# Performance work log

Measured on AMD Instinct MI355X. Metric: run time of the kernel, lower is better.

## Reference

```python
import jax, jax.numpy as jnp
import numpy as np

B, S, C, H, E, K = 8, 512, 768, 12, 8, 2
MLP_H = int(C * 4.0)
HD = C // H
ROUTER_REG = 0.01
LN_EPS = 1e-5


def setup_inputs() -> dict:
    key = jax.random.key(0)
    ks = jax.random.split(key, 8)

    def w(k, shape, fan_in):
        return (jax.random.normal(k, shape, dtype=jnp.float32) / np.sqrt(fan_in)).astype(jnp.float32)

    return {
        "x": jax.random.normal(ks[0], (B, S, C), dtype=jnp.float32),
        "expert_tokens": w(ks[1], (E, C), C),
        "ln1_g": jnp.ones((E, C), jnp.float32),
        "ln1_b": jnp.zeros((E, C), jnp.float32),
        "qkv_w": w(ks[2], (E, C, 3 * C), C),
        "qkv_b": jnp.zeros((E, 3 * C), jnp.float32),
        "proj_w": w(ks[3], (E, C, C), C),
        "proj_b": jnp.zeros((E, C), jnp.float32),
        "ln2_g": jnp.ones((E, C), jnp.float32),
        "ln2_b": jnp.zeros((E, C), jnp.float32),
        "fc1_w": w(ks[4], (E, C, MLP_H), C),
        "fc1_b": jnp.zeros((E, MLP_H), jnp.float32),
        "fc2_w": w(ks[5], (E, MLP_H, C), MLP_H),
        "fc2_b": jnp.zeros((E, C), jnp.float32),
    }


def _layernorm(x, g, b):
    mu = jnp.mean(x, axis=-1, keepdims=True)
    var = jnp.mean(jnp.square(x - mu), axis=-1, keepdims=True)
    return (x - mu) * jax.lax.rsqrt(var + LN_EPS) * g + b


def _block(x, p):
    # One transformer Block (pre-LN attention + MLP), params for a single expert.
    ln1_g, ln1_b, qkv_w, qkv_b, proj_w, proj_b, ln2_g, ln2_b, fc1_w, fc1_b, fc2_w, fc2_b = p
    h = _layernorm(x, ln1_g, ln1_b)
    qkv = (h @ qkv_w + qkv_b).reshape(B, S, 3, H, HD)
    q, k, v = qkv[:, :, 0], qkv[:, :, 1], qkv[:, :, 2]  # [B,S,H,HD]
    # NOTE: original code MULTIPLIES by sqrt(head_dim) (scale = head_dim**0.5).
    scale = jnp.float32(np.sqrt(HD))
    attn = jax.nn.softmax(jnp.einsum('bqhd,bkhd->bhqk', q, k) * scale, axis=-1)
    o = jnp.einsum('bhqk,bkhd->bqhd', attn, v).reshape(B, S, C)
    x = x + (o @ proj_w + proj_b)
    h2 = _layernorm(x, ln2_g, ln2_b)
    x = x + (jax.nn.gelu(h2 @ fc1_w + fc1_b, approximate=False) @ fc2_w + fc2_b)
    return x


def reference(x, expert_tokens, ln1_g, ln1_b, qkv_w, qkv_b, proj_w, proj_b,
              ln2_g, ln2_b, fc1_w, fc1_b, fc2_w, fc2_b):
    # Router
    router_logits = jnp.einsum('bsc,nc->bsn', x, expert_tokens) / jnp.float32(np.sqrt(C))
    router_probs = jax.nn.softmax(router_logits, axis=-1)
    top_k_probs, top_k_idx = jax.lax.top_k(router_probs, K)  # [B,S,K]
    top_k_probs = top_k_probs / jnp.sum(top_k_probs, axis=-1, keepdims=True)

    # Dense all-expert compute (sequential over experts to bound memory)
    params = (ln1_g, ln1_b, qkv_w, qkv_b, proj_w, proj_b, ln2_g, ln2_b,
              fc1_w, fc1_b, fc2_w, fc2_b)
    expert_out = jax.lax.map(lambda p: _block(x, p), params)  # [E,B,S,C]
    expert_out = jnp.transpose(expert_out, (1, 2, 0, 3))       # [B,S,E,C]

    # Top-k gather and weighted combine
    sel = jnp.take_along_axis(expert_out, top_k_idx[..., None], axis=2)  # [B,S,K,C]
    combine = jnp.sum(sel * top_k_probs[..., None], axis=2)
    out = x + combine

    # Load-balance auxiliary loss
    counts = jnp.sum(jax.nn.one_hot(top_k_idx, E, dtype=jnp.float32), axis=(0, 1, 2))
    f_i = counts / jnp.float32(B * S * K)
    P_i = jnp.mean(router_probs, axis=(0, 1))
    balance_loss = E * jnp.sum(f_i * P_i) + ROUTER_REG * jnp.linalg.norm(expert_tokens)
    return out, balance_loss
```

## Files before the change

### kernel.cpp

```cpp
#include <hip/hip_runtime.h>
#include <hip/hip_bf16.h>

#define BB 8
#define SS 512
#define CC 768
#define HH 12
#define HD 64
#define EE 8
#define KK 2
#define MLPH 3072
#define NT (BB*SS)
#define NOUT (NT*CC)

#define SLOTB      68059136ull
#define SLOT_U16   34029568ull
#define SLOT_F32   17014784ull

typedef unsigned int u32;
typedef unsigned short u16;
typedef __attribute__((ext_vector_type(8))) short short8;
typedef __attribute__((ext_vector_type(4))) float f32x4;

__device__ __forceinline__ u16 f2bf(float f) {
    u32 u = __builtin_bit_cast(u32, f);
    u32 r = (u + 0x7fffu + ((u >> 16) & 1u)) >> 16;
    return (u16)r;
}
__device__ __forceinline__ float bf2f(u16 h) {
    u32 u = ((u32)h) << 16;
    return __builtin_bit_cast(float, u);
}
__device__ __forceinline__ void gl_lds16(const void* g, void* l) {
    __builtin_amdgcn_global_load_lds(
        (const __attribute__((address_space(1))) u32*)g,
        (__attribute__((address_space(3))) u32*)l, 16, 0, 0);
}
__device__ __forceinline__ void swz_rc(int bid, int& bm, int& bn) {
    int xcd = bid & 7, off = bid >> 3;
    bm = (xcd * 4 + (off & 3)) * 128;
    bn = (off >> 2) * 128;
}

__device__ __forceinline__ void stage128x64(const u16* __restrict__ G, size_t ldg,
                                            u16* s, int tid)
{
    int wid = tid >> 6, lane = tid & 63;
#pragma unroll
    for (int it = 0; it < 4; ++it) {
        int cb = it * 256 + wid * 64;
        int c = cb + lane;
        int row = c >> 3;
        int ch = (c & 7) ^ (row & 7);
        gl_lds16(G + (size_t)row * ldg + ch * 8, s + cb * 8);
    }
}
__device__ __forceinline__ short8 frag64(const u16* s, int row, int kc, int lb) {
    int ch = (kc * 4 + lb) ^ (row & 7);
    return *(const short8*)(s + row * 64 + ch * 8);
}

__device__ __forceinline__ void stg_dp(const u16* __restrict__ A, const u16* __restrict__ B,
                                       int ldk, u16* sA, u16* sB, int t, int tid)
{
    int wid = tid >> 6, lane = tid & 63;
#pragma unroll
    for (int rd = 0; rd < 2; rd++) {
        int cb = rd * 256 + wid * 64;
        int c = cb + lane;
        gl_lds16(A + (size_t)(c >> 2) * ldk + t * 32 + (c & 3) * 8, sA + cb * 8);
    }
#pragma unroll
    for (int rd = 0; rd < 2; rd++) {
        int cb = rd * 256 + wid * 64;
        int c = cb + lane;
        gl_lds16(B + (size_t)(c >> 2) * ldk + t * 32 + (c & 3) * 8, sB + cb * 8);
    }
}

__global__ __launch_bounds__(256) void router_kernel(const float* __restrict__ x,
    const float* __restrict__ et, float* __restrict__ W, float* __restrict__ stats)
{
    __shared__ float etl[EE * CC];
    __shared__ float pred[4][2 * EE];
    int tid = threadIdx.x;
    for (int i = tid; i < EE * CC; i += 256) etl[i] = et[i];
    __syncthreads();
    int wid = tid >> 6, lane = tid & 63;
    float psum[EE] = {}, csum[EE] = {};
    for (int i = 0; i < 2; i++) {
        int t = blockIdx.x * 8 + wid * 2 + i;
        const float* xr = x + (size_t)t * CC;
        float acc[EE] = {};
        for (int c = lane; c < CC; c += 64) {
            float xv = xr[c];
#pragma unroll
            for (int e = 0; e < EE; e++) acc[e] += xv * etl[e * CC + c];
        }
#pragma unroll
        for (int e = 0; e < EE; e++)
            for (int off = 1; off < 64; off <<= 1) acc[e] += __shfl_xor(acc[e], off, 64);
        if (lane == 0) {
            const float inv = 0.03608439182435161f;
            float l[EE], m = -1e30f;
#pragma unroll
            for (int e = 0; e < EE; e++) { l[e] = acc[e] * inv; m = fmaxf(m, l[e]); }
            float p[EE], sum = 0.f;
#pragma unroll
            for (int e = 0; e < EE; e++) { p[e] = __expf(l[e] - m); sum += p[e]; }
            int i1 = 0;
#pragma unroll
            for (int e = 1; e < EE; e++) if (p[e] > p[i1]) i1 = e;
            int i2 = -1;
#pragma unroll
            for (int e = 0; e < EE; e++) if (e != i1 && (i2 < 0 || p[e] > p[i2])) i2 = e;
            float wn = p[i1] + p[i2];
#pragma unroll
            for (int e = 0; e < EE; e++) W[t * EE + e] = 0.f;
            W[t * EE + i1] = p[i1] / wn;
            W[t * EE + i2] = p[i2] / wn;
#pragma unroll
            for (int e = 0; e < EE; e++) psum[e] += p[e] / sum;
            csum[i1] += 1.f; csum[i2] += 1.f;
        }
    }
    if (lane == 0) {
#pragma unroll
        for (int e = 0; e < EE; e++) { pred[wid][e] = psum[e]; pred[wid][EE + e] = csum[e]; }
    }
    __syncthreads();
    if (tid < 2 * EE) {
        float s = pred[0][tid] + pred[1][tid] + pred[2][tid] + pred[3][tid];
        atomicAdd(&stats[tid], s);
    }
}

template<int MODE>
__global__ __launch_bounds__(256) void ln_kernel(const float* __restrict__ x, size_t xslot,
    u16* __restrict__ out_hi, u16* __restrict__ out_lo, size_t oslot)
{
    int t = blockIdx.x;
    int eb = blockIdx.y;
    const float* xr = x + (size_t)eb * xslot + (size_t)t * CC;
    __shared__ float red[256];
    int tid = threadIdx.x;
    float v[3];
    float s = 0.f;
#pragma unroll
    for (int i = 0; i < 3; i++) { v[i] = xr[tid + i * 256]; s += v[i]; }
    red[tid] = s; __syncthreads();
    for (int off = 128; off > 0; off >>= 1) { if (tid < off) red[tid] += red[tid + off]; __syncthreads(); }
    float mu = red[0] / (float)CC;
    __syncthreads();
    float s2 = 0.f;
#pragma unroll
    for (int i = 0; i < 3; i++) { float d = v[i] - mu; s2 += d * d; }
    red[tid] = s2; __syncthreads();
    for (int off = 128; off > 0; off >>= 1) { if (tid < off) red[tid] += red[tid + off]; __syncthreads(); }
    float var = red[0] / (float)CC;
    float sc = rsqrtf(var + 1e-5f);
#pragma unroll
    for (int i = 0; i < 3; i++) {
        int c = tid + i * 256;
        float val = (v[i] - mu) * sc;
        u16 hi = f2bf(val);
        out_hi[(size_t)eb * oslot + (size_t)t * CC + c] = hi;
        if (MODE) out_lo[(size_t)eb * oslot + (size_t)t * CC + c] = f2bf(val - bf2f(hi));
    }
}

__global__ __launch_bounds__(256) void prep_expert(
    const float* __restrict__ qkv_w0, const float* __restrict__ qkv_b0,
    const float* __restrict__ proj_w0,
    const float* __restrict__ fc1_w0, const float* __restrict__ fc1_b0,
    const float* __restrict__ fc2_w0,
    const float* __restrict__ g1_0, const float* __restrict__ b1_0,
    const float* __restrict__ g2_0, const float* __restrict__ b2_0,
    u16* __restrict__ qkvTh, u16* __restrict__ qkvTl,
    u16* __restrict__ projT, u16* __restrict__ fc1T, u16* __restrict__ fc2T,
    float* __restrict__ biasq, float* __restrict__ biasf1, int ebase)
{
    __shared__ float tile[32][33];
    __shared__ float bsh[CC];
    __shared__ float redg[256];
    int bid = blockIdx.x;
    int eb = blockIdx.y;
    int ge = ebase + eb;
    int tid = threadIdx.x;
    const float* qkv_w = qkv_w0 + (size_t)ge * CC * 3 * CC;
    const float* qkv_b = qkv_b0 + (size_t)ge * 3 * CC;
    const float* proj_w = proj_w0 + (size_t)ge * CC * CC;
    const float* fc1_w = fc1_w0 + (size_t)ge * CC * MLPH;
    const float* fc1_b = fc1_b0 + (size_t)ge * MLPH;
    const float* fc2_w = fc2_w0 + (size_t)ge * MLPH * CC;
    const float* g1 = g1_0 + (size_t)ge * CC;
    const float* b1 = b1_0 + (size_t)ge * CC;
    const float* g2 = g2_0 + (size_t)ge * CC;
    const float* b2 = b2_0 + (size_t)ge * CC;

    if (bid < 6912) {
        const float* src; const float* scale = nullptr;
        u16 *dh, *dl = nullptr; int N, Kd, n0, k0;
        if (bid < 1728) {
            src = qkv_w; scale = g1;
            dh = qkvTh + (size_t)eb * SLOT_U16; dl = qkvTl + (size_t)eb * SLOT_U16;
            N = 2304; Kd = 768; n0 = (bid % 72) * 32; k0 = (bid / 72) * 32;
        } else if (bid < 2304) {
            int i = bid - 1728;
            src = proj_w; dh = projT + (size_t)eb * SLOT_U16; N = 768; Kd = 768;
            n0 = (i % 24) * 32; k0 = (i / 24) * 32;
        } else if (bid < 4608) {
            int i = bid - 2304;
            src = fc1_w; scale = g2; dh = fc1T + (size_t)eb * SLOT_U16; N = 3072; Kd = 768;
            n0 = (i % 96) * 32; k0 = (i / 96) * 32;
        } else {
            int i = bid - 4608;
            src = fc2_w; dh = fc2T + (size_t)eb * SLOT_U16; N = 768; Kd = 3072;
            n0 = (i % 24) * 32; k0 = (i / 24) * 32;
        }
        int tx = tid & 31, ty = tid >> 5;
#pragma unroll
        for (int i = 0; i < 32; i += 8) {
            float v = src[(size_t)(k0 + ty + i) * N + n0 + tx];
            if (scale) v *= scale[k0 + ty + i];
            tile[ty + i][tx] = v;
        }
        __syncthreads();
#pragma unroll
        for (int i = 0; i < 32; i += 8) {
            float v = tile[tx][ty + i];
            u16 hi = f2bf(v);
            dh[(size_t)(n0 + ty + i) * Kd + k0 + tx] = hi;
            if (dl) dl[(size_t)(n0 + ty + i) * Kd + k0 + tx] = f2bf(v - bf2f(hi));
        }
    } else {
        const float* bv; const float* wsrc; const float* badd;
        float* dst; int N, n0;
        if (bid < 6984) { bv = b1; wsrc = qkv_w; badd = qkv_b; dst = biasq + (size_t)eb * SLOT_F32; N = 2304; n0 = (bid - 6912) * 32; }
        else            { bv = b2; wsrc = fc1_w; badd = fc1_b; dst = biasf1 + (size_t)eb * SLOT_F32; N = MLPH; n0 = (bid - 6984) * 32; }
        for (int i = tid; i < CC; i += 256) bsh[i] = bv[i];
        __syncthreads();
        int g = tid & 31, l8 = tid >> 5;
        int n = n0 + g;
        float acc = 0.f;
        for (int k = l8; k < CC; k += 8) acc += bsh[k] * wsrc[(size_t)k * N + n];
        redg[tid] = acc; __syncthreads();
        if (tid < 32) {
            float sum = 0.f;
#pragma unroll
            for (int i = 0; i < 8; i++) sum += redg[tid + i * 32];
            dst[n0 + tid] = sum + badd[n0 + tid];
        }
    }
}

__global__ __launch_bounds__(256) void gemm_qkv_bk64(
    const u16* __restrict__ Ah, const u16* __restrict__ Al,
    const u16* __restrict__ Bh0, const u16* __restrict__ Bl0,
    const float* __restrict__ biasq0, u16* __restrict__ qk_hi0,
    u16* __restrict__ qk_lo0, u16* __restrict__ vtout0)
{
    __shared__ __align__(16) u16 sAh[128 * 64], sAl[128 * 64];
    __shared__ __align__(16) u16 sBh[128 * 64], sBl[128 * 64];
    int tid = threadIdx.x;
    int eb = blockIdx.y;
    int bm, bn;
    swz_rc(blockIdx.x, bm, bn);
    bool qk_tile = (bn < 1536);
    int wid = tid >> 6, lane = tid & 63;
    int wr = wid >> 1, wc = wid & 1;
    int la = lane & 15, lb = lane >> 4;
    const u16* Bh = Bh0 + (size_t)eb * SLOT_U16;
    const u16* Bl = Bl0 + (size_t)eb * SLOT_U16;
    const float* bias = biasq0 + (size_t)eb * SLOT_F32;
    u16* qk_hi = qk_hi0 + (size_t)eb * SLOT_U16;
    u16* qk_lo = qk_lo0 + (size_t)eb * SLOT_U16;
    u16* vtout = vtout0 + (size_t)eb * SLOT_U16;

    f32x4 acc[4][4];
#pragma unroll
    for (int i = 0; i < 4; i++)
#pragma unroll
        for (int j = 0; j < 4; j++) acc[i][j] = (f32x4){0.f, 0.f, 0.f, 0.f};

    const u16* Abh = Ah + (size_t)bm * CC;
    const u16* Abl = Al + (size_t)bm * CC;
    const u16* Bbh = Bh + (size_t)bn * CC;
    const u16* Bbl = Bl + (size_t)bn * CC;
    for (int k0 = 0; k0 < CC; k0 += 64) {
        stage128x64(Abh + k0, CC, sAh, tid);
        stage128x64(Bbh + k0, CC, sBh, tid);
        if (qk_tile) {
            stage128x64(Abl + k0, CC, sAl, tid);
            stage128x64(Bbl + k0, CC, sBl, tid);
        }
        __syncthreads();
        if (qk_tile) {
#pragma unroll
            for (int kc = 0; kc < 2; kc++) {
                short8 avh[4], avl[4], bvh[4], bvl[4];
#pragma unroll
                for (int i = 0; i < 4; i++) {
                    int row = wr * 64 + i * 16 + la;
                    avh[i] = frag64(sAh, row, kc, lb);
                    avl[i] = frag64(sAl, row, kc, lb);
                }
#pragma unroll
                for (int j = 0; j < 4; j++) {
                    int row = wc * 64 + j * 16 + la;
                    bvh[j] = frag64(sBh, row, kc, lb);
                    bvl[j] = frag64(sBl, row, kc, lb);
                }
#pragma unroll
                for (int i = 0; i < 4; i++)
#pragma unroll
                    for (int j = 0; j < 4; j++) {
                        acc[i][j] = __builtin_amdgcn_mfma_f32_16x16x32_bf16(avh[i], bvh[j], acc[i][j], 0, 0, 0);
                        acc[i][j] = __builtin_amdgcn_mfma_f32_16x16x32_bf16(avh[i], bvl[j], acc[i][j], 0, 0, 0);
                        acc[i][j] = __builtin_amdgcn_mfma_f32_16x16x32_bf16(avl[i], bvh[j], acc[i][j], 0, 0, 0);
                    }
            }
        } else {
#pragma unroll
            for (int kc = 0; kc < 2; kc++) {
                short8 avh[4], bvh[4];
#pragma unroll
                for (int i = 0; i < 4; i++) avh[i] = frag64(sAh, wr * 64 + i * 16 + la, kc, lb);
#pragma unroll
                for (int j = 0; j < 4; j++) bvh[j] = frag64(sBh, wc * 64 + j * 16 + la, kc, lb);
#pragma unroll
                for (int i = 0; i < 4; i++)
#pragma unroll
                    for (int j = 0; j < 4; j++)
                        acc[i][j] = __builtin_amdgcn_mfma_f32_16x16x32_bf16(avh[i], bvh[j], acc[i][j], 0, 0, 0);
            }
        }
        __syncthreads();
    }
#pragma unroll
    for (int i = 0; i < 4; i++) {
#pragma unroll
        for (int j = 0; j < 4; j++) {
            int gn = bn + wc * 64 + j * 16 + la;
            float bsv = bias[gn];
#pragma unroll
            for (int r = 0; r < 4; r++) {
                int gm = bm + wr * 64 + i * 16 + lb * 4 + r;
                float v = acc[i][j][r] + bsv;
                if (gn < 1536) {
                    u16 hi = f2bf(v);
                    qk_hi[(size_t)gm * 1536 + gn] = hi;
                    qk_lo[(size_t)gm * 1536 + gn] = f2bf(v - bf2f(hi));
                } else {
                    int dd = (gn - 1536) & 63, hh = (gn - 1536) >> 6;
                    int ss = gm & (SS - 1), bb = gm >> 9;
                    vtout[((size_t)((bb * HH + hh) * HD + dd)) * SS + ss] = f2bf(v);
                }
            }
        }
    }
}

__global__ __launch_bounds__(256) void gemm_proj(
    const u16* __restrict__ A, const u16* __restrict__ BT,
    const float* __restrict__ bias0, const float* __restrict__ x,
    float* __restrict__ Cout)
{
    __shared__ __align__(16) u16 sA[128 * 64];
    __shared__ __align__(16) u16 sB[128 * 64];
    int tid = threadIdx.x;
    int eb = blockIdx.y;
    int bm, bn;
    swz_rc(blockIdx.x, bm, bn);
    int wid = tid >> 6, lane = tid & 63;
    int wr = wid >> 1, wc = wid & 1;
    int la = lane & 15, lb = lane >> 4;
    f32x4 acc[4][4];
#pragma unroll
    for (int i = 0; i < 4; i++)
#pragma unroll
        for (int j = 0; j < 4; j++) acc[i][j] = (f32x4){0.f, 0.f, 0.f, 0.f};

    const u16* Ab = A + (size_t)eb * SLOT_U16 + (size_t)bm * CC;
    const u16* Bb = BT + (size_t)eb * SLOT_U16 + (size_t)bn * CC;
    for (int k0 = 0; k0 < CC; k0 += 64) {
        stage128x64(Ab + k0, CC, sA, tid);
        stage128x64(Bb + k0, CC, sB, tid);
        __syncthreads();
#pragma unroll
        for (int kc = 0; kc < 2; kc++) {
            short8 av[4], bv[4];
#pragma unroll
            for (int i = 0; i < 4; i++) av[i] = frag64(sA, wr * 64 + i * 16 + la, kc, lb);
#pragma unroll
            for (int j = 0; j < 4; j++) bv[j] = frag64(sB, wc * 64 + j * 16 + la, kc, lb);
#pragma unroll
            for (int i = 0; i < 4; i++)
#pragma unroll
                for (int j = 0; j < 4; j++)
                    acc[i][j] = __builtin_amdgcn_mfma_f32_16x16x32_bf16(av[i], bv[j], acc[i][j], 0, 0, 0);
        }
        __syncthreads();
    }
    const float* biasp = bias0 + (size_t)eb * CC;
    float* C = Cout + (size_t)eb * SLOT_F32;
#pragma unroll
    for (int i = 0; i < 4; i++) {
#pragma unroll
        for (int j = 0; j < 4; j++) {
            int gn = bn + wc * 64 + j * 16 + la;
            float bsv = biasp[gn];
#pragma unroll
            for (int r = 0; r < 4; r++) {
                int gm = bm + wr * 64 + i * 16 + lb * 4 + r;
                size_t idx = (size_t)gm * CC + gn;
                C[idx] = x[idx] + acc[i][j][r] + bsv;
            }
        }
    }
}

template<int EPI>
__device__ __forceinline__ void gemm_dp_body(
    const u16* __restrict__ Ab, const u16* __restrict__ Bb, int Kdim,
    const float* __restrict__ biasp, const float* __restrict__ resp,
    const float* __restrict__ Wt, int ge, const float* __restrict__ xinit,
    void* __restrict__ Cout, int N, int bm, int bn)
{
    __shared__ __align__(16) u16 sA[3][128 * 32];
    __shared__ __align__(16) u16 sB[3][128 * 32];
    int tid = threadIdx.x;
    int wid = tid >> 6, lane = tid & 63;
    int wr = wid >> 1, wc = wid & 1;
    int la = lane & 15, lb = lane >> 4;
    int NTILE = Kdim / 32;

    f32x4 acc[4][4];
#pragma unroll
    for (int i = 0; i < 4; i++)
#pragma unroll
        for (int j = 0; j < 4; j++) acc[i][j] = (f32x4){0.f, 0.f, 0.f, 0.f};

    stg_dp(Ab, Bb, Kdim, sA[0], sB[0], 0, tid);
    stg_dp(Ab, Bb, Kdim, sA[1], sB[1], 1, tid);

    for (int t = 0; t < NTILE; t++) {
        if (t < NTILE - 1) asm volatile("s_waitcnt vmcnt(4)" ::: "memory");
        else               asm volatile("s_waitcnt vmcnt(0)" ::: "memory");
        asm volatile("" ::: "memory");
        __builtin_amdgcn_s_barrier();
        asm volatile("" ::: "memory");

        const u16* cA = &sA[t % 3][0];
        const u16* cB = &sB[t % 3][0];
        __builtin_amdgcn_s_setprio(1);
        short8 bv[4];
#pragma unroll
        for (int j = 0; j < 4; j++)
            bv[j] = *(const short8*)(cB + ((size_t)(wc * 64 + j * 16 + la) * 4 + lb) * 8);
#pragma unroll
        for (int i = 0; i < 4; i++) {
            short8 av = *(const short8*)(cA + ((size_t)(wr * 64 + i * 16 + la) * 4 + lb) * 8);
#pragma unroll
            for (int j = 0; j < 4; j++)
                acc[i][j] = __builtin_amdgcn_mfma_f32_16x16x32_bf16(av, bv[j], acc[i][j], 0, 0, 0);
        }
        __builtin_amdgcn_s_setprio(0);

        if (t + 2 < NTILE) stg_dp(Ab, Bb, Kdim, sA[(t + 2) % 3], sB[(t + 2) % 3], t + 2, tid);
    }

#pragma unroll
    for (int i = 0; i < 4; i++) {
#pragma unroll
        for (int j = 0; j < 4; j++) {
            int gn = bn + wc * 64 + j * 16 + la;
            float bsv = biasp[gn];
#pragma unroll
            for (int r = 0; r < 4; r++) {
                int gm = bm + wr * 64 + i * 16 + lb * 4 + r;
                size_t idx = (size_t)gm * N + gn;
                float v = acc[i][j][r] + bsv;
                if (EPI == 2) {
                    float gel = 0.5f * v * (1.0f + erff(v * 0.70710678118654752f));
                    ((u16*)Cout)[idx] = f2bf(gel);
                } else {
                    float w = Wt[(size_t)gm * EE + ge];
                    float val = w * (v + resp[idx]);
                    if (ge == 0) val += xinit[idx];
                    atomicAdd(&((float*)Cout)[idx], val);
                }
            }
        }
    }
}

__global__ __launch_bounds__(256) void gemm_fc1_dp(
    const u16* __restrict__ A0, const u16* __restrict__ BT0,
    const float* __restrict__ bias0, u16* __restrict__ C0)
{
    int eb = blockIdx.y;
    int bm, bn;
    swz_rc(blockIdx.x, bm, bn);
    gemm_dp_body<2>(A0 + (size_t)eb * SLOT_U16 + (size_t)bm * CC,
                    BT0 + (size_t)eb * SLOT_U16 + (size_t)bn * CC, CC,
                    bias0 + (size_t)eb * SLOT_F32, nullptr, nullptr, 0, nullptr,
                    C0 + (size_t)eb * SLOT_U16, MLPH, bm, bn);
}

__global__ __launch_bounds__(256) void gemm_fc2_dp(
    const u16* __restrict__ A0, const u16* __restrict__ BT0,
    const float* __restrict__ bias0, const float* __restrict__ res0,
    const float* __restrict__ Wt, int ebase, const float* __restrict__ xinit,
    float* __restrict__ Cout)
{
    int eb = blockIdx.y;
    int bm, bn;
    swz_rc(blockIdx.x, bm, bn);
    gemm_dp_body<5>(A0 + (size_t)eb * SLOT_U16 + (size_t)bm * MLPH,
                    BT0 + (size_t)eb * SLOT_U16 + (size_t)bn * MLPH, MLPH,
                    bias0 + (size_t)eb * CC, res0 + (size_t)eb * SLOT_F32,
                    Wt, ebase + eb, xinit, Cout, CC, bm, bn);
}

__global__ __launch_bounds__(256) void attn_mfma(const u16* __restrict__ qk_hi0,
    const u16* __restrict__ qk_lo0, const u16* __restrict__ vt0, u16* __restrict__ o0)
{
    int q0 = blockIdx.x * 64;
    int h = blockIdx.y;
    int z = blockIdx.z;
    int b = z & (BB - 1), eb = z >> 3;
    int tid = threadIdx.x, wid = tid >> 6, lane = tid & 63;
    int la = lane & 15, lb = lane >> 4;
    __shared__ __align__(16) u16 Ksh[64 * 64];
    __shared__ __align__(16) u16 Ksl[64 * 64];
    __shared__ __align__(16) u16 Vs[64 * 64];
    __shared__ __align__(16) u16 Ps[4][16 * 64];

    const u16* qk_hi = qk_hi0 + (size_t)eb * SLOT_U16;
    const u16* qk_lo = qk_lo0 + (size_t)eb * SLOT_U16;
    const u16* vt = vt0 + (size_t)eb * SLOT_U16;
    u16* o = o0 + (size_t)eb * SLOT_U16;

    short8 aqh[2], aql[2];
    {
        size_t qoff = (size_t)(b * SS + q0 + wid * 16 + la) * 1536 + h * HD;
#pragma unroll
        for (int kc = 0; kc < 2; kc++) {
            aqh[kc] = *(const short8*)(qk_hi + qoff + kc * 32 + lb * 8);
            aql[kc] = *(const short8*)(qk_lo + qoff + kc * 32 + lb * 8);
        }
    }
    const u16* kbh = qk_hi + (size_t)(b * SS) * 1536 + CC + h * HD;
    const u16* kbl = qk_lo + (size_t)(b * SS) * 1536 + CC + h * HD;
    const u16* vtbase = vt + (size_t)((b * HH + h) * HD) * SS;

    float m_r[4], l_r[4];
    f32x4 acc_o[4];
#pragma unroll
    for (int r = 0; r < 4; r++) { m_r[r] = -1e30f; l_r[r] = 0.f; }
#pragma unroll
    for (int d0 = 0; d0 < 4; d0++) acc_o[d0] = (f32x4){0.f, 0.f, 0.f, 0.f};

    for (int kt = 0; kt < SS; kt += 64) {
#pragma unroll
        for (int it = 0; it < 2; it++) {
            int base = it * 256 + wid * 64;
            int c = base + lane;
            int row = c >> 3;
            int gk = (c & 7) ^ (row & 7);
            gl_lds16(kbh + (size_t)(kt + row) * 1536 + gk * 8, Ksh + base * 8);
            gl_lds16(kbl + (size_t)(kt + row) * 1536 + gk * 8, Ksl + base * 8);
            gl_lds16(vtbase + (size_t)row * SS + kt + gk * 8, Vs + base * 8);
        }
        __syncthreads();

        f32x4 s4[4];
#pragma unroll
        for (int j = 0; j < 4; j++) s4[j] = (f32x4){0.f, 0.f, 0.f, 0.f};
#pragma unroll
        for (int kc = 0; kc < 2; kc++)
#pragma unroll
            for (int j = 0; j < 4; j++) {
                size_t off = (size_t)(j * 16 + la) * 64 + (((kc * 4 + lb) ^ (la & 7)) * 8);
                short8 bkh = *(const short8*)(Ksh + off);
                short8 bkl = *(const short8*)(Ksl + off);
                s4[j] = __builtin_amdgcn_mfma_f32_16x16x32_bf16(aqh[kc], bkh, s4[j], 0, 0, 0);
                s4[j] = __builtin_amdgcn_mfma_f32_16x16x32_bf16(aql[kc], bkh, s4[j], 0, 0, 0);
                s4[j] = __builtin_amdgcn_mfma_f32_16x16x32_bf16(aqh[kc], bkl, s4[j], 0, 0, 0);
            }
#pragma unroll
        for (int j = 0; j < 4; j++) s4[j] = s4[j] * 8.f;

#pragma unroll
        for (int r = 0; r < 4; r++) {
            float mx = fmaxf(fmaxf(s4[0][r], s4[1][r]), fmaxf(s4[2][r], s4[3][r]));
#pragma unroll
            for (int off = 1; off < 16; off <<= 1) mx = fmaxf(mx, __shfl_xor(mx, off, 64));
            float mn = fmaxf(m_r[r], mx);
            float corr = __expf(m_r[r] - mn);
            m_r[r] = mn;
            float rs = 0.f;
#pragma unroll
            for (int j = 0; j < 4; j++) {
                float p = __expf(s4[j][r] - mn);
                s4[j][r] = p; rs += p;
            }
#pragma unroll
            for (int off = 1; off < 16; off <<= 1) rs += __shfl_xor(rs, off, 64);
            l_r[r] = l_r[r] * corr + rs;
#pragma unroll
            for (int d0 = 0; d0 < 4; d0++) acc_o[d0][r] = acc_o[d0][r] * corr;
        }
#pragma unroll
        for (int j = 0; j < 4; j++)
#pragma unroll
            for (int r = 0; r < 4; r++) {
                int row = lb * 4 + r;
                int sg = (2 * j + (la >> 3)) ^ (row & 7);
                Ps[wid][row * 64 + sg * 8 + (la & 7)] = f2bf(s4[j][r]);
            }
        short8 pa[2];
#pragma unroll
        for (int kc = 0; kc < 2; kc++)
            pa[kc] = *(const short8*)(&Ps[wid][la * 64 + (((kc * 4 + lb) ^ (la & 7)) * 8)]);
#pragma unroll
        for (int d0 = 0; d0 < 4; d0++)
#pragma unroll
            for (int kc = 0; kc < 2; kc++) {
                short8 bv = *(const short8*)(&Vs[(d0 * 16 + la) * 64 + (((kc * 4 + lb) ^ (la & 7)) * 8)]);
                acc_o[d0] = __builtin_amdgcn_mfma_f32_16x16x32_bf16(pa[kc], bv, acc_o[d0], 0, 0, 0);
            }
        __syncthreads();
    }
#pragma unroll
    for (int r = 0; r < 4; r++) {
        float invl = 1.f / l_r[r];
        int tok = b * SS + q0 + wid * 16 + lb * 4 + r;
#pragma unroll
        for (int d0 = 0; d0 < 4; d0++)
            o[(size_t)tok * CC + h * HD + d0 * 16 + la] = f2bf(acc_o[d0][r] * invl);
    }
}

__global__ __launch_bounds__(256) void loss_kernel(const float* __restrict__ et,
    const float* __restrict__ stats, float* __restrict__ out_loss)
{
    __shared__ float red[256];
    int tid = threadIdx.x;
    float s = 0.f;
    for (int i = tid; i < EE * CC; i += 256) { float v = et[i]; s += v * v; }
    red[tid] = s; __syncthreads();
    for (int off = 128; off > 0; off >>= 1) { if (tid < off) red[tid] += red[tid + off]; __syncthreads(); }
    if (tid == 0) {
        float bl = 0.f;
        for (int e = 0; e < EE; e++) {
            float f = stats[EE + e] / (float)(NT * KK);
            float P = stats[e] / (float)NT;
            bl += f * P;
        }
        *out_loss = (float)EE * bl + 0.01f * sqrtf(red[0]);
    }
}

extern "C" void kernel_launch(void* const* d_in, const int* in_sizes, int n_in,
                              void* d_out, int out_size, void* d_ws, size_t ws_size,
                              hipStream_t stream) {
    const float* x      = (const float*)d_in[0];
    const float* et     = (const float*)d_in[1];
    const float* ln1_g  = (const float*)d_in[2];
    const float* ln1_b  = (const float*)d_in[3];
    const float* qkv_w  = (const float*)d_in[4];
    const float* qkv_b  = (const float*)d_in[5];
    const float* proj_w = (const float*)d_in[6];
    const float* proj_b = (const float*)d_in[7];
    const float* ln2_g  = (const float*)d_in[8];
    const float* ln2_b  = (const float*)d_in[9];
    const float* fc1_w  = (const float*)d_in[10];
    const float* fc1_b  = (const float*)d_in[11];
    const float* fc2_w  = (const float*)d_in[12];
    const float* fc2_b  = (const float*)d_in[13];
    float* outp = (float*)d_out;
    char* base = (char*)d_ws;

    const size_t FIXED = 12714496;
    int EB = 1;
    if (ws_size >= FIXED + 8 * SLOTB) EB = 8;
    else if (ws_size >= FIXED + 4 * SLOTB) EB = 4;
    else if (ws_size >= FIXED + 2 * SLOTB) EB = 2;

    float* W      = (float*)(base);
    float* stats  = (float*)(base + 131072);
    u16*   xh_hi  = (u16*)  (base + 131584);
    u16*   xh_lo  = (u16*)  (base + 6423040);
    char* slot0 = base + FIXED;
    u16*   qkvTh  = (u16*)  (slot0);
    u16*   qkvTl  = (u16*)  (slot0 + 3538944);
    u16*   projT  = (u16*)  (slot0 + 7077888);
    u16*   fc1T   = (u16*)  (slot0 + 8257536);
    u16*   fc2T   = (u16*)  (slot0 + 12976128);
    float* biasq  = (float*)(slot0 + 17694720);
    float* biasf1 = (float*)(slot0 + 17711104);
    u16*   qk_hi  = (u16*)  (slot0 + 17727488);
    u16*   qk_lo  = (u16*)  (slot0 + 30310400);
    u16*   mlp1   = (u16*)  (slot0 + 17727488);
    u16*   vtb    = (u16*)  (slot0 + 42893312);
    u16*   xmhat  = (u16*)  (slot0 + 42893312);
    u16*   obf    = (u16*)  (slot0 + 49184768);
    float* xmid   = (float*)(slot0 + 55476224);

    hipMemsetAsync(stats, 0, 16 * sizeof(float), stream);
    hipMemsetAsync(outp, 0, (size_t)NOUT * sizeof(float), stream);

    router_kernel<<<NT / 8, 256, 0, stream>>>(x, et, W, stats);
    ln_kernel<1><<<dim3(NT, 1), 256, 0, stream>>>(x, 0, xh_hi, xh_lo, 0);

    for (int ebase = 0; ebase < EE; ebase += EB) {
        prep_expert<<<dim3(7080, EB), 256, 0, stream>>>(
            qkv_w, qkv_b, proj_w, fc1_w, fc1_b, fc2_w,
            ln1_g, ln1_b, ln2_g, ln2_b,
            qkvTh, qkvTl, projT, fc1T, fc2T, biasq, biasf1, ebase);

        gemm_qkv_bk64<<<dim3(18 * 32, EB), 256, 0, stream>>>(
            xh_hi, xh_lo, qkvTh, qkvTl, biasq, qk_hi, qk_lo, vtb);

        attn_mfma<<<dim3(SS / 64, HH, BB * EB), 256, 0, stream>>>(qk_hi, qk_lo, vtb, obf);

        gemm_proj<<<dim3(6 * 32, EB), 256, 0, stream>>>(
            obf, projT, proj_b + (size_t)ebase * CC, x, xmid);

        ln_kernel<0><<<dim3(NT, EB), 256, 0, stream>>>(xmid, SLOT_F32, xmhat, nullptr, SLOT_U16);

        gemm_fc1_dp<<<dim3(24 * 32, EB), 256, 0, stream>>>(xmhat, fc1T, biasf1, mlp1);

        gemm_fc2_dp<<<dim3(6 * 32, EB), 256, 0, stream>>>(
            mlp1, fc2T, fc2_b + (size_t)ebase * CC, xmid, W, ebase, x, outp);
    }

    loss_kernel<<<1, 256, 0, stream>>>(et, stats, outp + NOUT);
}
```

Baseline: 1.448 ms.

## Pipeline QKV and proj GEMMs with triple-buffered async LDS staging

Replaces the single-buffered BK=64 QKV GEMM with a three-stage BK=32 pipeline using global_load_lds and vmcnt waits. B tiles are staged in LDS, while A fragments (hi/lo) are read directly from global memory into registers. The proj GEMM is moved onto the shared pipelined gemm_dp_body through a new EPI==1 residual epilogue. This aims to overlap loads with MFMA work and remove the per-tile double barrier, at the cost of uncached direct global reads for A, which are repeated across column tiles.

```diff
diff --git a/kernel.cpp b/kernel.cpp
--- a/kernel.cpp
+++ b/kernel.cpp
@@ -39,24 +39,6 @@
     int xcd = bid & 7, off = bid >> 3;
     bm = (xcd * 4 + (off & 3)) * 128;
     bn = (off >> 2) * 128;
-}
-
-__device__ __forceinline__ void stage128x64(const u16* __restrict__ G, size_t ldg,
-                                            u16* s, int tid)
-{
-    int wid = tid >> 6, lane = tid & 63;
-#pragma unroll
-    for (int it = 0; it < 4; ++it) {
-        int cb = it * 256 + wid * 64;
-        int c = cb + lane;
-        int row = c >> 3;
-        int ch = (c & 7) ^ (row & 7);
-        gl_lds16(G + (size_t)row * ldg + ch * 8, s + cb * 8);
-    }
-}
-__device__ __forceinline__ short8 frag64(const u16* s, int row, int kc, int lb) {
-    int ch = (kc * 4 + lb) ^ (row & 7);
-    return *(const short8*)(s + row * 64 + ch * 8);
 }
 
 __device__ __forceinline__ void stg_dp(const u16* __restrict__ A, const u16* __restrict__ B,
@@ -253,89 +235,106 @@
     }
 }
 
-__global__ __launch_bounds__(256) void gemm_qkv_bk64(
+__global__ __launch_bounds__(256) void gemm_qkv_dp(
     const u16* __restrict__ Ah, const u16* __restrict__ Al,
     const u16* __restrict__ Bh0, const u16* __restrict__ Bl0,
     const float* __restrict__ biasq0, u16* __restrict__ qk_hi0,
     u16* __restrict__ qk_lo0, u16* __restrict__ vtout0)
 {
-    __shared__ __align__(16) u16 sAh[128 * 64], sAl[128 * 64];
-    __shared__ __align__(16) u16 sBh[128 * 64], sBl[128 * 64];
+    __shared__ __align__(16) u16 sBh[3][128 * 32];
+    __shared__ __align__(16) u16 sBl[3][128 * 32];
+    const int NTILE = CC / 32;
     int tid = threadIdx.x;
     int eb = blockIdx.y;
     int bm, bn;
     swz_rc(blockIdx.x, bm, bn);
-    bool qk_tile = (bn < 1536);
+    bool qk = (bn < 1536);
     int wid = tid >> 6, lane = tid & 63;
     int wr = wid >> 1, wc = wid & 1;
     int la = lane & 15, lb = lane >> 4;
-    const u16* Bh = Bh0 + (size_t)eb * SLOT_U16;
-    const u16* Bl = Bl0 + (size_t)eb * SLOT_U16;
+
+    const u16* Bh = Bh0 + (size_t)eb * SLOT_U16 + (size_t)bn * CC;
+    const u16* Bl = Bl0 + (size_t)eb * SLOT_U16 + (size_t)bn * CC;
+    const u16* Ahb = Ah + (size_t)bm * CC;
+    const u16* Alb = Al + (size_t)bm * CC;
+
+    auto STG = [&](int s, int t) {
+#pragma unroll
+        for (int rd = 0; rd < 2; rd++) {
+            int cb = rd * 256 + wid * 64;
+            int c = cb + lane;
+            gl_lds16(Bh + (size_t)(c >> 2) * CC + t * 32 + (c & 3) * 8, &sBh[s][(size_t)cb * 8]);
+        }
+        if (qk) {
+#pragma unroll
+            for (int rd = 0; rd < 2; rd++) {
+                int cb = rd * 256 + wid * 64;
+                int c = cb + lane;
+                gl_lds16(Bl + (size_t)(c >> 2) * CC + t * 32 + (c & 3) * 8, &sBl[s][(size_t)cb * 8]);
+            }
+        }
+    };
+
+    f32x4 acc[4][4];
+#pragma unroll
+    for (int i = 0; i < 4; i++)
+#pragma unroll
+        for (int j = 0; j < 4; j++) acc[i][j] = (f32x4){0.f, 0.f, 0.f, 0.f};
+
+    STG(0, 0);
+    STG(1, 1);
+
+    for (int t = 0; t < NTILE; t++) {
+        if (t < NTILE - 1) {
+            if (qk) asm volatile("s_waitcnt vmcnt(4)" ::: "memory");
+            else    asm volatile("s_waitcnt vmcnt(2)" ::: "memory");
+        } else {
+            asm volatile("s_waitcnt vmcnt(0)" ::: "memory");
+        }
+        __builtin_amdgcn_s_barrier();
+        asm volatile("" ::: "memory");
+
+        short8 avh[4], avl[4];
+#pragma unroll
+        for (int i = 0; i < 4; i++)
+            avh[i] = *(const short8*)(Ahb + (size_t)(wr * 64 + i * 16 + la) * CC + t * 32 + lb * 8);
+        if (qk) {
+#pragma unroll
+            for (int i = 0; i < 4; i++)
+                avl[i] = *(const short8*)(Alb + (size_t)(wr * 64 + i * 16 + la) * CC + t * 32 + lb * 8);
+        }
+
+        const u16* cBh = &sBh[t % 3][0];
+        const u16* cBl = &sBl[t % 3][0];
+        __builtin_amdgcn_s_setprio(1);
+#pragma unroll
+        for (int j = 0; j < 4; j++) {
+            short8 bvh = *(const short8*)(cBh + (size_t)(wc * 64 + j * 16 + la) * 32 + lb * 8);
+#pragma unroll
+            for (int i = 0; i < 4; i++)
+                acc[i][j] = __builtin_amdgcn_mfma_f32_16x16x32_bf16(avh[i], bvh, acc[i][j], 0, 0, 0);
+        }
+        if (qk) {
+#pragma unroll
+            for (int j = 0; j < 4; j++) {
+                short8 bvh = *(const short8*)(cBh + (size_t)(wc * 64 + j * 16 + la) * 32 + lb * 8);
+                short8 bvl = *(const short8*)(cBl + (size_t)(wc * 64 + j * 16 + la) * 32 + lb * 8);
+#pragma unroll
+                for (int i = 0; i < 4; i++) {
+                    acc[i][j] = __builtin_amdgcn_mfma_f32_16x16x32_bf16(avh[i], bvl, acc[i][j], 0, 0, 0);
+                    acc[i][j] = __builtin_amdgcn_mfma_f32_16x16x32_bf16(avl[i], bvh, acc[i][j], 0, 0, 0);
+                }
+            }
+        }
+        __builtin_amdgcn_s_setprio(0);
+
+        if (t + 2 < NTILE) STG((t + 2) % 3, t + 2);
+    }
+
     const float* bias = biasq0 + (size_t)eb * SLOT_F32;
     u16* qk_hi = qk_hi0 + (size_t)eb * SLOT_U16;
     u16* qk_lo = qk_lo0 + (size_t)eb * SLOT_U16;
     u16* vtout = vtout0 + (size_t)eb * SLOT_U16;
-
-    f32x4 acc[4][4];
-#pragma unroll
-    for (int i = 0; i < 4; i++)
-#pragma unroll
-        for (int j = 0; j < 4; j++) acc[i][j] = (f32x4){0.f, 0.f, 0.f, 0.f};
-
-    const u16* Abh = Ah + (size_t)bm * CC;
-    const u16* Abl = Al + (size_t)bm * CC;
-    const u16* Bbh = Bh + (size_t)bn * CC;
-    const u16* Bbl = Bl + (size_t)bn * CC;
-    for (int k0 = 0; k0 < CC; k0 += 64) {
-        stage128x64(Abh + k0, CC, sAh, tid);
-        stage128x64(Bbh + k0, CC, sBh, tid);
-        if (qk_tile) {
-            stage128x64(Abl + k0, CC, sAl, tid);
-            stage128x64(Bbl + k0, CC, sBl, tid);
-        }
-        __syncthreads();
-        if (qk_tile) {
-#pragma unroll
-            for (int kc = 0; kc < 2; kc++) {
-                short8 avh[4], avl[4], bvh[4], bvl[4];
-#pragma unroll
-                for (int i = 0; i < 4; i++) {
-                    int row = wr * 64 + i * 16 + la;
-                    avh[i] = frag64(sAh, row, kc, lb);
-                    avl[i] = frag64(sAl, row, kc, lb);
-                }
-#pragma unroll
-                for (int j = 0; j < 4; j++) {
-                    int row = wc * 64 + j * 16 + la;
-                    bvh[j] = frag64(sBh, row, kc, lb);
-                    bvl[j] = frag64(sBl, row, kc, lb);
-                }
-#pragma unroll
-                for (int i = 0; i < 4; i++)
-#pragma unroll
-                    for (int j = 0; j < 4; j++) {
-                        acc[i][j] = __builtin_amdgcn_mfma_f32_16x16x32_bf16(avh[i], bvh[j], acc[i][j], 0, 0, 0);
-                        acc[i][j] = __builtin_amdgcn_mfma_f32_16x16x32_bf16(avh[i], bvl[j], acc[i][j], 0, 0, 0);
-                        acc[i][j] = __builtin_amdgcn_mfma_f32_16x16x32_bf16(avl[i], bvh[j], acc[i][j], 0, 0, 0);
-                    }
-            }
-        } else {
-#pragma unroll
-            for (int kc = 0; kc < 2; kc++) {
-                short8 avh[4], bvh[4];
-#pragma unroll
-                for (int i = 0; i < 4; i++) avh[i] = frag64(sAh, wr * 64 + i * 16 + la, kc, lb);
-#pragma unroll
-                for (int j = 0; j < 4; j++) bvh[j] = frag64(sBh, wc * 64 + j * 16 + la, kc, lb);
-#pragma unroll
-                for (int i = 0; i < 4; i++)
-#pragma unroll
-                    for (int j = 0; j < 4; j++)
-                        acc[i][j] = __builtin_amdgcn_mfma_f32_16x16x32_bf16(avh[i], bvh[j], acc[i][j], 0, 0, 0);
-            }
-        }
-        __syncthreads();
-    }
 #pragma unroll
     for (int i = 0; i < 4; i++) {
 #pragma unroll
@@ -360,65 +359,6 @@
     }
 }
 
-__global__ __launch_bounds__(256) void gemm_proj(
-    const u16* __restrict__ A, const u16* __restrict__ BT,
-    const float* __restrict__ bias0, const float* __restrict__ x,
-    float* __restrict__ Cout)
-{
-    __shared__ __align__(16) u16 sA[128 * 64];
-    __shared__ __align__(16) u16 sB[128 * 64];
-    int tid = threadIdx.x;
-    int eb = blockIdx.y;
-    int bm, bn;
-    swz_rc(blockIdx.x, bm, bn);
-    int wid = tid >> 6, lane = tid & 63;
-    int wr = wid >> 1, wc = wid & 1;
-    int la = lane & 15, lb = lane >> 4;
-    f32x4 acc[4][4];
-#pragma unroll
-    for (int i = 0; i < 4; i++)
-#pragma unroll
-        for (int j = 0; j < 4; j++) acc[i][j] = (f32x4){0.f, 0.f, 0.f, 0.f};
-
-    const u16* Ab = A + (size_t)eb * SLOT_U16 + (size_t)bm * CC;
-    const u16* Bb = BT + (size_t)eb * SLOT_U16 + (size_t)bn * CC;
-    for (int k0 = 0; k0 < CC; k0 += 64) {
-        stage128x64(Ab + k0, CC, sA, tid);
-        stage128x64(Bb + k0, CC, sB, tid);
-        __syncthreads();
-#pragma unroll
-        for (int kc = 0; kc < 2; kc++) {
-            short8 av[4], bv[4];
-#pragma unroll
-            for (int i = 0; i < 4; i++) av[i] = frag64(sA, wr * 64 + i * 16 + la, kc, lb);
-#pragma unroll
-            for (int j = 0; j < 4; j++) bv[j] = frag64(sB, wc * 64 + j * 16 + la, kc, lb);
-#pragma unroll
-            for (int i = 0; i < 4; i++)
-#pragma unroll
-                for (int j = 0; j < 4; j++)
-                    acc[i][j] = __builtin_amdgcn_mfma_f32_16x16x32_bf16(av[i], bv[j], acc[i][j], 0, 0, 0);
-        }
-        __syncthreads();
-    }
-    const float* biasp = bias0 + (size_t)eb * CC;
-    float* C = Cout + (size_t)eb * SLOT_F32;
-#pragma unroll
-    for (int i = 0; i < 4; i++) {
-#pragma unroll
-        for (int j = 0; j < 4; j++) {
-            int gn = bn + wc * 64 + j * 16 + la;
-            float bsv = biasp[gn];
-#pragma unroll
-            for (int r = 0; r < 4; r++) {
-                int gm = bm + wr * 64 + i * 16 + lb * 4 + r;
-                size_t idx = (size_t)gm * CC + gn;
-                C[idx] = x[idx] + acc[i][j][r] + bsv;
-            }
-        }
-    }
-}
-
 template<int EPI>
 __device__ __forceinline__ void gemm_dp_body(
     const u16* __restrict__ Ab, const u16* __restrict__ Bb, int Kdim,
@@ -446,7 +386,6 @@
     for (int t = 0; t < NTILE; t++) {
         if (t < NTILE - 1) asm volatile("s_waitcnt vmcnt(4)" ::: "memory");
         else               asm volatile("s_waitcnt vmcnt(0)" ::: "memory");
-        asm volatile("" ::: "memory");
         __builtin_amdgcn_s_barrier();
         asm volatile("" ::: "memory");
 
@@ -480,7 +419,9 @@
                 int gm = bm + wr * 64 + i * 16 + lb * 4 + r;
                 size_t idx = (size_t)gm * N + gn;
                 float v = acc[i][j][r] + bsv;
-                if (EPI == 2) {
+                if (EPI == 1) {
+                    ((float*)Cout)[idx] = resp[idx] + v;
+                } else if (EPI == 2) {
                     float gel = 0.5f * v * (1.0f + erff(v * 0.70710678118654752f));
                     ((u16*)Cout)[idx] = f2bf(gel);
                 } else {
@@ -492,6 +433,20 @@
             }
         }
     }
+}
+
+__global__ __launch_bounds__(256) void gemm_proj_dp(
+    const u16* __restrict__ A0, const u16* __restrict__ BT0,
+    const float* __restrict__ bias0, const float* __restrict__ x,
+    float* __restrict__ C0)
+{
+    int eb = blockIdx.y;
+    int bm, bn;
+    swz_rc(blockIdx.x, bm, bn);
+    gemm_dp_body<1>(A0 + (size_t)eb * SLOT_U16 + (size_t)bm * CC,
+                    BT0 + (size_t)eb * SLOT_U16 + (size_t)bn * CC, CC,
+                    bias0 + (size_t)eb * CC, x, nullptr, 0, nullptr,
+                    C0 + (size_t)eb * SLOT_F32, CC, bm, bn);
 }
 
 __global__ __launch_bounds__(256) void gemm_fc1_dp(
@@ -720,12 +675,12 @@
             ln1_g, ln1_b, ln2_g, ln2_b,
             qkvTh, qkvTl, projT, fc1T, fc2T, biasq, biasf1, ebase);
 
-        gemm_qkv_bk64<<<dim3(18 * 32, EB), 256, 0, stream>>>(
+        gemm_qkv_dp<<<dim3(18 * 32, EB), 256, 0, stream>>>(
             xh_hi, xh_lo, qkvTh, qkvTl, biasq, qk_hi, qk_lo, vtb);
 
         attn_mfma<<<dim3(SS / 64, HH, BB * EB), 256, 0, stream>>>(qk_hi, qk_lo, vtb, obf);
 
-        gemm_proj<<<dim3(6 * 32, EB), 256, 0, stream>>>(
+        gemm_proj_dp<<<dim3(6 * 32, EB), 256, 0, stream>>>(
             obf, projT, proj_b + (size_t)ebase * CC, x, xmid);
 
         ln_kernel<0><<<dim3(NT, EB), 256, 0, stream>>>(xmid, SLOT_F32, xmhat, nullptr, SLOT_U16);
```

Measured after the change: 1.595 ms. +10.2%, slower.

## Write V row-major then transpose via LDS kernel; use pipelined GEMM for proj

Applied to the files above, without the earlier changes.

The QKV GEMM epilogue now writes V in plain row-major layout instead of scattering 2-byte stores into a transposed layout. A new LDS-tiled kernel then produces the transposed V that attention reads. The proj GEMM moves onto the triple-buffered gemm_dp_body with a new residual-add epilogue, and one compiler barrier is dropped from the pipelined loop. The aim is to replace uncoalesced strided stores and to speed up proj, at the cost of an extra kernel launch and an extra pass over V (vraw reuses the obf buffer).

```diff
diff --git a/kernel.cpp b/kernel.cpp
--- a/kernel.cpp
+++ b/kernel.cpp
@@ -257,7 +257,7 @@
     const u16* __restrict__ Ah, const u16* __restrict__ Al,
     const u16* __restrict__ Bh0, const u16* __restrict__ Bl0,
     const float* __restrict__ biasq0, u16* __restrict__ qk_hi0,
-    u16* __restrict__ qk_lo0, u16* __restrict__ vtout0)
+    u16* __restrict__ qk_lo0, u16* __restrict__ vraw0)
 {
     __shared__ __align__(16) u16 sAh[128 * 64], sAl[128 * 64];
     __shared__ __align__(16) u16 sBh[128 * 64], sBl[128 * 64];
@@ -274,7 +274,7 @@
     const float* bias = biasq0 + (size_t)eb * SLOT_F32;
     u16* qk_hi = qk_hi0 + (size_t)eb * SLOT_U16;
     u16* qk_lo = qk_lo0 + (size_t)eb * SLOT_U16;
-    u16* vtout = vtout0 + (size_t)eb * SLOT_U16;
+    u16* vraw = vraw0 + (size_t)eb * SLOT_U16;
 
     f32x4 acc[4][4];
 #pragma unroll
@@ -351,71 +351,42 @@
                     qk_hi[(size_t)gm * 1536 + gn] = hi;
                     qk_lo[(size_t)gm * 1536 + gn] = f2bf(v - bf2f(hi));
                 } else {
-                    int dd = (gn - 1536) & 63, hh = (gn - 1536) >> 6;
-                    int ss = gm & (SS - 1), bb = gm >> 9;
-                    vtout[((size_t)((bb * HH + hh) * HD + dd)) * SS + ss] = f2bf(v);
+                    vraw[(size_t)gm * CC + (gn - 1536)] = f2bf(v);
                 }
             }
         }
     }
 }
 
-__global__ __launch_bounds__(256) void gemm_proj(
-    const u16* __restrict__ A, const u16* __restrict__ BT,
-    const float* __restrict__ bias0, const float* __restrict__ x,
-    float* __restrict__ Cout)
-{
-    __shared__ __align__(16) u16 sA[128 * 64];
-    __shared__ __align__(16) u16 sB[128 * 64];
+__global__ __launch_bounds__(256) void vtrans(const u16* __restrict__ vraw0,
+    u16* __restrict__ vt0)
+{
+    __shared__ u16 tile[64][65];
+    int st = blockIdx.x;
+    int h = blockIdx.y;
+    int z = blockIdx.z;
+    int b = z & (BB - 1), eb = z >> 3;
+    const u16* vraw = vraw0 + (size_t)eb * SLOT_U16;
+    u16* vt = vt0 + (size_t)eb * SLOT_U16;
     int tid = threadIdx.x;
-    int eb = blockIdx.y;
-    int bm, bn;
-    swz_rc(blockIdx.x, bm, bn);
-    int wid = tid >> 6, lane = tid & 63;
-    int wr = wid >> 1, wc = wid & 1;
-    int la = lane & 15, lb = lane >> 4;
-    f32x4 acc[4][4];
-#pragma unroll
-    for (int i = 0; i < 4; i++)
-#pragma unroll
-        for (int j = 0; j < 4; j++) acc[i][j] = (f32x4){0.f, 0.f, 0.f, 0.f};
-
-    const u16* Ab = A + (size_t)eb * SLOT_U16 + (size_t)bm * CC;
-    const u16* Bb = BT + (size_t)eb * SLOT_U16 + (size_t)bn * CC;
-    for (int k0 = 0; k0 < CC; k0 += 64) {
-        stage128x64(Ab + k0, CC, sA, tid);
-        stage128x64(Bb + k0, CC, sB, tid);
-        __syncthreads();
-#pragma unroll
-        for (int kc = 0; kc < 2; kc++) {
-            short8 av[4], bv[4];
-#pragma unroll
-            for (int i = 0; i < 4; i++) av[i] = frag64(sA, wr * 64 + i * 16 + la, kc, lb);
-#pragma unroll
-            for (int j = 0; j < 4; j++) bv[j] = frag64(sB, wc * 64 + j * 16 + la, kc, lb);
-#pragma unroll
-            for (int i = 0; i < 4; i++)
-#pragma unroll
-                for (int j = 0; j < 4; j++)
-                    acc[i][j] = __builtin_amdgcn_mfma_f32_16x16x32_bf16(av[i], bv[j], acc[i][j], 0, 0, 0);
-        }
-        __syncthreads();
-    }
-    const float* biasp = bias0 + (size_t)eb * CC;
-    float* C = Cout + (size_t)eb * SLOT_F32;
-#pragma unroll
-    for (int i = 0; i < 4; i++) {
-#pragma unroll
-        for (int j = 0; j < 4; j++) {
-            int gn = bn + wc * 64 + j * 16 + la;
-            float bsv = biasp[gn];
-#pragma unroll
-            for (int r = 0; r < 4; r++) {
-                int gm = bm + wr * 64 + i * 16 + lb * 4 + r;
-                size_t idx = (size_t)gm * CC + gn;
-                C[idx] = x[idx] + acc[i][j][r] + bsv;
-            }
-        }
+    int row = tid >> 3, ch = tid & 7;
+#pragma unroll
+    for (int it = 0; it < 2; it++) {
+        int s = it * 32 + row;
+        const u16* src = vraw + (size_t)(b * SS + st * 64 + s) * CC + h * HD + ch * 8;
+        short8 v = *(const short8*)src;
+#pragma unroll
+        for (int k = 0; k < 8; k++) tile[s][ch * 8 + k] = (u16)v[k];
+    }
+    __syncthreads();
+#pragma unroll
+    for (int it = 0; it < 2; it++) {
+        int d = it * 32 + row;
+        u16* dst = vt + ((size_t)((b * HH + h) * HD + d)) * SS + st * 64 + ch * 8;
+        short8 v;
+#pragma unroll
+        for (int k = 0; k < 8; k++) v[k] = (short)tile[ch * 8 + k][d];
+        *(short8*)dst = v;
     }
 }
 
@@ -446,7 +417,6 @@
     for (int t = 0; t < NTILE; t++) {
         if (t < NTILE - 1) asm volatile("s_waitcnt vmcnt(4)" ::: "memory");
         else               asm volatile("s_waitcnt vmcnt(0)" ::: "memory");
-        asm volatile("" ::: "memory");
         __builtin_amdgcn_s_barrier();
         asm volatile("" ::: "memory");
 
@@ -480,7 +450,9 @@
                 int gm = bm + wr * 64 + i * 16 + lb * 4 + r;
                 size_t idx = (size_t)gm * N + gn;
                 float v = acc[i][j][r] + bsv;
-                if (EPI == 2) {
+                if (EPI == 1) {
+                    ((float*)Cout)[idx] = resp[idx] + v;
+                } else if (EPI == 2) {
                     float gel = 0.5f * v * (1.0f + erff(v * 0.70710678118654752f));
                     ((u16*)Cout)[idx] = f2bf(gel);
                 } else {
@@ -492,6 +464,20 @@
             }
         }
     }
+}
+
+__global__ __launch_bounds__(256) void gemm_proj_dp(
+    const u16* __restrict__ A0, const u16* __restrict__ BT0,
+    const float* __restrict__ bias0, const float* __restrict__ x,
+    float* __restrict__ C0)
+{
+    int eb = blockIdx.y;
+    int bm, bn;
+    swz_rc(blockIdx.x, bm, bn);
+    gemm_dp_body<1>(A0 + (size_t)eb * SLOT_U16 + (size_t)bm * CC,
+                    BT0 + (size_t)eb * SLOT_U16 + (size_t)bn * CC, CC,
+                    bias0 + (size_t)eb * CC, x, nullptr, 0, nullptr,
+                    C0 + (size_t)eb * SLOT_F32, CC, bm, bn);
 }
 
 __global__ __launch_bounds__(256) void gemm_fc1_dp(
@@ -706,6 +692,7 @@
     u16*   vtb    = (u16*)  (slot0 + 42893312);
     u16*   xmhat  = (u16*)  (slot0 + 42893312);
     u16*   obf    = (u16*)  (slot0 + 49184768);
+    u16*   vraw   = obf;
     float* xmid   = (float*)(slot0 + 55476224);
 
     hipMemsetAsync(stats, 0, 16 * sizeof(float), stream);
@@ -721,11 +708,13 @@
             qkvTh, qkvTl, projT, fc1T, fc2T, biasq, biasf1, ebase);
 
         gemm_qkv_bk64<<<dim3(18 * 32, EB), 256, 0, stream>>>(
-            xh_hi, xh_lo, qkvTh, qkvTl, biasq, qk_hi, qk_lo, vtb);
+            xh_hi, xh_lo, qkvTh, qkvTl, biasq, qk_hi, qk_lo, vraw);
+
+        vtrans<<<dim3(SS / 64, HH, BB * EB), 256, 0, stream>>>(vraw, vtb);
 
         attn_mfma<<<dim3(SS / 64, HH, BB * EB), 256, 0, stream>>>(qk_hi, qk_lo, vtb, obf);
 
-        gemm_proj<<<dim3(6 * 32, EB), 256, 0, stream>>>(
+        gemm_proj_dp<<<dim3(6 * 32, EB), 256, 0, stream>>>(
             obf, projT, proj_b + (size_t)ebase * CC, x, xmid);
 
         ln_kernel<0><<<dim3(NT, EB), 256, 0, stream>>>(xmid, SLOT_F32, xmhat, nullptr, SLOT_U16);
```

Result: no change. 1.427 ms (median of 2 runs) (-1.4%).
